# Optimization experiments

Measured on AMD Instinct MI355X. Metric: run time of the kernel, lower is better.

Reference implementation:

```python
import jax, jax.numpy as jnp
import numpy as np

B, S, K, N, G = 4, 16, 8192, 8192, 128
NUM_GROUPS = K // G

def setup_inputs() -> dict:
    key = jax.random.key(0)
    k1, k2, k3, k4, k5 = jax.random.split(key, 5)
    x = jax.random.normal(k1, (B, S, K), dtype=jnp.float32)
    qweight = jax.random.randint(k2, (K, N), -128, 128, dtype=jnp.int32)
    # small positive scales like real quantizers produce
    scales = jax.random.uniform(k3, (NUM_GROUPS, N), dtype=jnp.float32) * 0.01 + 1e-4
    zeros = jax.random.uniform(k4, (NUM_GROUPS, N), dtype=jnp.float32) * 2.0 - 1.0
    bias = jax.random.normal(k5, (N,), dtype=jnp.float32)
    return {"x": x, "qweight": qweight, "scales": scales, "zeros": zeros,
            "bias": bias, "group_size": G}

def reference(x, qweight, scales, zeros, bias, group_size):
    # Expand per-group scale/zero along K: [num_groups, N] -> [K, N]
    Kdim = qweight.shape[0]
    if scales.shape[0] == 1:
        scale_exp = jnp.broadcast_to(scales, (Kdim, scales.shape[1]))
        zero_exp = jnp.broadcast_to(zeros, (Kdim, zeros.shape[1]))
    else:
        scale_exp = jnp.repeat(scales, group_size, axis=0)[:Kdim]
        zero_exp = jnp.repeat(zeros, group_size, axis=0)[:Kdim]
    # Dequantize: W[k, n] = (q - zero) * scale
    weight_fp = (qweight.astype(x.dtype) - zero_exp) * scale_exp  # [K, N]
    out = jnp.einsum('bsk,kn->bsn', x, weight_fp) + bias
    return out
```

## Files before the change

kernel.cpp:

```cpp
#include <hip/hip_runtime.h>

typedef __attribute__((ext_vector_type(8))) short short8;
typedef __attribute__((ext_vector_type(8))) unsigned short ushort8;
typedef __attribute__((ext_vector_type(4))) unsigned short ushort4v;
typedef __attribute__((ext_vector_type(4))) int int4v;
typedef __attribute__((ext_vector_type(4))) float f32x4;

#define Mdim 64
#define Kdim 8192
#define Ndim 8192
#define GRP 128
#define NGRP 64
#define KSPLIT 8
#define NG2 (NGRP / KSPLIT)
#define BN 128

#define SWZ(row, kk) ((row)*128 + ((kk) ^ (8*((((row) >> 3) ^ (row)) & 7))))

__device__ __forceinline__ unsigned short f2bf(float f) {
    unsigned int u = __builtin_bit_cast(unsigned int, f);
    u += 0x7FFFu + ((u >> 16) & 1u);
    return (unsigned short)(u >> 16);
}
__device__ __forceinline__ float bf2f(unsigned short h) {
    unsigned int u = ((unsigned int)h) << 16;
    return __builtin_bit_cast(float, u);
}

__global__ void prep_kernel(const float* __restrict__ x,
                            unsigned short* __restrict__ xh,
                            unsigned short* __restrict__ xl,
                            float* __restrict__ xsum) {
    const int tid = threadIdx.x;
    const int u = blockIdx.x * 8 + (tid >> 5);
    const int g = u & (NGRP - 1);
    const int m = u >> 6;
    const int lane = tid & 31;
    const int k = g * GRP + lane * 4;
    f32x4 v = *(const f32x4*)(x + (size_t)m * Kdim + k);
    ushort4v hv, lv;
    float s = 0.f;
#pragma unroll
    for (int i = 0; i < 4; ++i) {
        unsigned short h = f2bf(v[i]);
        hv[i] = h;
        lv[i] = f2bf(v[i] - bf2f(h));
        s += v[i];
    }
    *(ushort4v*)(xh + (size_t)m * Kdim + k) = hv;
    *(ushort4v*)(xl + (size_t)m * Kdim + k) = lv;
#pragma unroll
    for (int off = 16; off > 0; off >>= 1) s += __shfl_down(s, off, 32);
    if (lane == 0) xsum[g * Mdim + m] = s;
}

__launch_bounds__(512, 4)
__global__ void qlin_kernel(const unsigned short* __restrict__ xh,
                            const unsigned short* __restrict__ xl,
                            const int* __restrict__ qw,
                            const float* __restrict__ scales,
                            const float* __restrict__ zeros,
                            const float* __restrict__ xsum,
                            float* __restrict__ pout) {
    __shared__ unsigned short lq[128 * 128];
    __shared__ unsigned short lxh[64 * 128];
    __shared__ unsigned short lxl[64 * 128];
    __shared__ float ls[NG2][128];
    __shared__ float lz[NG2][128];
    __shared__ float lxs[NG2][64];

    const int tid = threadIdx.x;
    const int kh = blockIdx.x & (KSPLIT - 1);
    const int n0 = (blockIdx.x >> 3) * BN;
    const int g0 = kh * NG2;
    const int ph = ((blockIdx.x >> 8) & 1) * (NG2 / 2);

    const int w = tid >> 6;
    const int l = tid & 63;
    const int lcol = l & 15;
    const int lhi = l >> 4;
    const int mt = (w >> 2) * 32;
    const int ns = (w & 3) * 32;

    const int qc = tid & 31;
    const int qr = tid >> 5;
    const int xc = tid & 15;
    const int xm = tid >> 4;

    const int c0 = n0 + ns + lcol;
    const int c1 = c0 + 16;

    int4v qv[8];
    ushort8 xga, xgb, xgc, xgd;

    auto LOADX = [&](int g) {
        const size_t kb = (size_t)g * GRP + xc * 8;
        xga = *(const ushort8*)(xh + (size_t)xm * Kdim + kb);
        xgb = *(const ushort8*)(xh + (size_t)(xm + 32) * Kdim + kb);
        xgc = *(const ushort8*)(xl + (size_t)xm * Kdim + kb);
        xgd = *(const ushort8*)(xl + (size_t)(xm + 32) * Kdim + kb);
    };
    auto LOADQ = [&](int g) {
        const size_t kb = (size_t)g * GRP + qr * 8;
        const int nc = n0 + qc * 4;
#pragma unroll
        for (int j = 0; j < 8; ++j)
            qv[j] = *(const int4v*)(qw + (kb + j) * Ndim + nc);
    };
    auto WRITEX = [&]() {
        *(ushort8*)&lxh[SWZ(xm, xc * 8)] = xga;
        *(ushort8*)&lxh[SWZ(xm + 32, xc * 8)] = xgb;
        *(ushort8*)&lxl[SWZ(xm, xc * 8)] = xgc;
        *(ushort8*)&lxl[SWZ(xm + 32, xc * 8)] = xgd;
    };
    auto WRITEQ = [&]() {
#pragma unroll
        for (int i = 0; i < 4; ++i) {
            int4v pk;
#pragma unroll
            for (int t = 0; t < 4; ++t) {
                unsigned lo = __builtin_bit_cast(unsigned, (float)qv[2 * t][i]) >> 16;
                unsigned hi = __builtin_bit_cast(unsigned, (float)qv[2 * t + 1][i]) & 0xFFFF0000u;
                pk[t] = (int)(lo | hi);
            }
            *(int4v*)&lq[SWZ(qc * 4 + i, qr * 8)] = pk;
        }
    };

    f32x4 acc00 = {0,0,0,0}, acc01 = {0,0,0,0}, acc10 = {0,0,0,0}, acc11 = {0,0,0,0};

    if (tid < 256) {
        *(f32x4*)&ls[tid >> 5][(tid & 31) * 4] =
            *(const f32x4*)(scales + (size_t)(g0 + (tid >> 5)) * Ndim + n0 + (tid & 31) * 4);
    } else {
        const int t = tid - 256;
        *(f32x4*)&lz[t >> 5][(t & 31) * 4] =
            *(const f32x4*)(zeros + (size_t)(g0 + (t >> 5)) * Ndim + n0 + (t & 31) * 4);
    }
    lxs[tid >> 6][tid & 63] = xsum[(g0 + (tid >> 6)) * Mdim + (tid & 63)];
    {
        const int ga = g0 + ph;
        LOADX(ga);
        LOADQ(ga);
        WRITEX();
        WRITEQ();
        __syncthreads();
    }

    for (int g = 0; g < NG2; ++g) {
        const int gi = (g + ph) & (NG2 - 1);
        const bool more = (g + 1 < NG2);

        if (more) {
            const int ga = g0 + ((g + 1 + ph) & (NG2 - 1));
            LOADX(ga);
            LOADQ(ga);
        }

        f32x4 p00 = {0,0,0,0}, p01 = {0,0,0,0}, p10 = {0,0,0,0}, p11 = {0,0,0,0};
#pragma unroll
        for (int ks = 0; ks < 4; ++ks) {
            const int kk = ks * 32 + lhi * 8;
            short8 bq0 = *(const short8*)&lq[SWZ(ns + lcol, kk)];
            short8 bq1 = *(const short8*)&lq[SWZ(ns + 16 + lcol, kk)];
            short8 ah0 = *(const short8*)&lxh[SWZ(mt + lcol, kk)];
            short8 al0 = *(const short8*)&lxl[SWZ(mt + lcol, kk)];
            short8 ah1 = *(const short8*)&lxh[SWZ(mt + 16 + lcol, kk)];
            short8 al1 = *(const short8*)&lxl[SWZ(mt + 16 + lcol, kk)];
            p00 = __builtin_amdgcn_mfma_f32_16x16x32_bf16(ah0, bq0, p00, 0, 0, 0);
            p00 = __builtin_amdgcn_mfma_f32_16x16x32_bf16(al0, bq0, p00, 0, 0, 0);
            p01 = __builtin_amdgcn_mfma_f32_16x16x32_bf16(ah0, bq1, p01, 0, 0, 0);
            p01 = __builtin_amdgcn_mfma_f32_16x16x32_bf16(al0, bq1, p01, 0, 0, 0);
            p10 = __builtin_amdgcn_mfma_f32_16x16x32_bf16(ah1, bq0, p10, 0, 0, 0);
            p10 = __builtin_amdgcn_mfma_f32_16x16x32_bf16(al1, bq0, p10, 0, 0, 0);
            p11 = __builtin_amdgcn_mfma_f32_16x16x32_bf16(ah1, bq1, p11, 0, 0, 0);
            p11 = __builtin_amdgcn_mfma_f32_16x16x32_bf16(al1, bq1, p11, 0, 0, 0);
        }
        {
            const float s0 = ls[gi][ns + lcol],      z0 = lz[gi][ns + lcol];
            const float s1 = ls[gi][ns + 16 + lcol], z1 = lz[gi][ns + 16 + lcol];
            f32x4 xs0 = *(const f32x4*)&lxs[gi][mt + lhi * 4];
            f32x4 xs1 = *(const f32x4*)&lxs[gi][mt + 16 + lhi * 4];
#pragma unroll
            for (int r = 0; r < 4; ++r) {
                acc00[r] += s0 * (p00[r] - z0 * xs0[r]);
                acc01[r] += s1 * (p01[r] - z1 * xs0[r]);
                acc10[r] += s0 * (p10[r] - z0 * xs1[r]);
                acc11[r] += s1 * (p11[r] - z1 * xs1[r]);
            }
        }

        if (more) {
            __syncthreads();
            WRITEX();
            WRITEQ();
            __syncthreads();
        }
    }

    const size_t ob = (size_t)kh * Mdim * Ndim;
#pragma unroll
    for (int r = 0; r < 4; ++r) {
        pout[ob + (size_t)(mt + lhi * 4 + r) * Ndim + c0] = acc00[r];
        pout[ob + (size_t)(mt + lhi * 4 + r) * Ndim + c1] = acc01[r];
        pout[ob + (size_t)(mt + 16 + lhi * 4 + r) * Ndim + c0] = acc10[r];
        pout[ob + (size_t)(mt + 16 + lhi * 4 + r) * Ndim + c1] = acc11[r];
    }
}

__global__ void reduce_kernel(const float* __restrict__ pout,
                              const float* __restrict__ bias,
                              float* __restrict__ out) {
    const size_t e = ((size_t)blockIdx.x * 256 + threadIdx.x) * 4;
    const int n = (int)(e & (Ndim - 1));
    f32x4 a = *(const f32x4*)(bias + n);
#pragma unroll
    for (int s = 0; s < KSPLIT; ++s) {
        f32x4 ppart = *(const f32x4*)(pout + (size_t)s * Mdim * Ndim + e);
#pragma unroll
        for (int r = 0; r < 4; ++r) a[r] += ppart[r];
    }
    *(f32x4*)(out + e) = a;
}

extern "C" void kernel_launch(void* const* d_in, const int* in_sizes, int n_in,
                              void* d_out, int out_size, void* d_ws, size_t ws_size,
                              hipStream_t stream) {
    const float* x = (const float*)d_in[0];
    const int* qw = (const int*)d_in[1];
    const float* scales = (const float*)d_in[2];
    const float* zeros = (const float*)d_in[3];
    const float* bias = (const float*)d_in[4];

    unsigned short* xh = (unsigned short*)d_ws;
    unsigned short* xl = xh + (size_t)Mdim * Kdim;
    float* xsum = (float*)(xl + (size_t)Mdim * Kdim);
    float* pout = xsum + NGRP * Mdim;
    float* out = (float*)d_out;

    prep_kernel<<<512, 256, 0, stream>>>(x, xh, xl, xsum);
    qlin_kernel<<<(Ndim / BN) * KSPLIT, 512, 0, stream>>>(xh, xl, qw, scales, zeros, xsum, pout);
    reduce_kernel<<<(Mdim * Ndim / 4) / 256, 256, 0, stream>>>(pout, bias, out);
}
```

Baseline: 61.53 us.

## Double-buffer LDS tiles with two-ahead prefetch and halve K-split

Shared-memory tiles for quantized weights and x hi/lo are now double-buffered, so each group step needs one barrier instead of two. Global loads for group g+2 are issued while group g+1 is written to the alternate buffer. KSPLIT drops from 8 to 4, which halves the partial-output traffic and the reduce work but gives each block twice as many K groups and half as many blocks. The per-block staggered start phase is removed, and launch bounds drop to 2 blocks per CU because LDS use roughly doubles, reducing occupancy.

```diff
diff --git a/kernel.cpp b/kernel.cpp
--- a/kernel.cpp
+++ b/kernel.cpp
@@ -11,7 +11,7 @@
 #define Ndim 8192
 #define GRP 128
 #define NGRP 64
-#define KSPLIT 8
+#define KSPLIT 4
 #define NG2 (NGRP / KSPLIT)
 #define BN 128
 
@@ -54,7 +54,7 @@
     if (lane == 0) xsum[g * Mdim + m] = s;
 }
 
-__launch_bounds__(512, 4)
+__launch_bounds__(512, 2)
 __global__ void qlin_kernel(const unsigned short* __restrict__ xh,
                             const unsigned short* __restrict__ xl,
                             const int* __restrict__ qw,
@@ -62,18 +62,17 @@
                             const float* __restrict__ zeros,
                             const float* __restrict__ xsum,
                             float* __restrict__ pout) {
-    __shared__ unsigned short lq[128 * 128];
-    __shared__ unsigned short lxh[64 * 128];
-    __shared__ unsigned short lxl[64 * 128];
+    __shared__ unsigned short lq[2][128 * 128];
+    __shared__ unsigned short lxh[2][64 * 128];
+    __shared__ unsigned short lxl[2][64 * 128];
     __shared__ float ls[NG2][128];
     __shared__ float lz[NG2][128];
     __shared__ float lxs[NG2][64];
 
     const int tid = threadIdx.x;
     const int kh = blockIdx.x & (KSPLIT - 1);
-    const int n0 = (blockIdx.x >> 3) * BN;
+    const int n0 = (blockIdx.x >> 2) * BN;
     const int g0 = kh * NG2;
-    const int ph = ((blockIdx.x >> 8) & 1) * (NG2 / 2);
 
     const int w = tid >> 6;
     const int l = tid & 63;
@@ -107,13 +106,13 @@
         for (int j = 0; j < 8; ++j)
             qv[j] = *(const int4v*)(qw + (kb + j) * Ndim + nc);
     };
-    auto WRITEX = [&]() {
-        *(ushort8*)&lxh[SWZ(xm, xc * 8)] = xga;
-        *(ushort8*)&lxh[SWZ(xm + 32, xc * 8)] = xgb;
-        *(ushort8*)&lxl[SWZ(xm, xc * 8)] = xgc;
-        *(ushort8*)&lxl[SWZ(xm + 32, xc * 8)] = xgd;
-    };
-    auto WRITEQ = [&]() {
+    auto WRITEX = [&](int b) {
+        *(ushort8*)&lxh[b][SWZ(xm, xc * 8)] = xga;
+        *(ushort8*)&lxh[b][SWZ(xm + 32, xc * 8)] = xgb;
+        *(ushort8*)&lxl[b][SWZ(xm, xc * 8)] = xgc;
+        *(ushort8*)&lxl[b][SWZ(xm + 32, xc * 8)] = xgd;
+    };
+    auto WRITEQ = [&](int b) {
 #pragma unroll
         for (int i = 0; i < 4; ++i) {
             int4v pk;
@@ -123,50 +122,44 @@
                 unsigned hi = __builtin_bit_cast(unsigned, (float)qv[2 * t + 1][i]) & 0xFFFF0000u;
                 pk[t] = (int)(lo | hi);
             }
-            *(int4v*)&lq[SWZ(qc * 4 + i, qr * 8)] = pk;
+            *(int4v*)&lq[b][SWZ(qc * 4 + i, qr * 8)] = pk;
         }
     };
 
     f32x4 acc00 = {0,0,0,0}, acc01 = {0,0,0,0}, acc10 = {0,0,0,0}, acc11 = {0,0,0,0};
 
-    if (tid < 256) {
-        *(f32x4*)&ls[tid >> 5][(tid & 31) * 4] =
-            *(const f32x4*)(scales + (size_t)(g0 + (tid >> 5)) * Ndim + n0 + (tid & 31) * 4);
-    } else {
-        const int t = tid - 256;
-        *(f32x4*)&lz[t >> 5][(t & 31) * 4] =
-            *(const f32x4*)(zeros + (size_t)(g0 + (t >> 5)) * Ndim + n0 + (t & 31) * 4);
-    }
-    lxs[tid >> 6][tid & 63] = xsum[(g0 + (tid >> 6)) * Mdim + (tid & 63)];
     {
-        const int ga = g0 + ph;
-        LOADX(ga);
-        LOADQ(ga);
-        WRITEX();
-        WRITEQ();
-        __syncthreads();
+        const int tg = tid >> 5, tc = tid & 31;
+        f32x4 sv = *(const f32x4*)(scales + (size_t)(g0 + tg) * Ndim + n0 + tc * 4);
+        f32x4 zv = *(const f32x4*)(zeros + (size_t)(g0 + tg) * Ndim + n0 + tc * 4);
+        float x0 = xsum[(g0 + (tid >> 6)) * Mdim + (tid & 63)];
+        float x1 = xsum[(g0 + ((tid + 512) >> 6)) * Mdim + (tid & 63)];
+        LOADX(g0);
+        LOADQ(g0);
+        *(f32x4*)&ls[tg][tc * 4] = sv;
+        *(f32x4*)&lz[tg][tc * 4] = zv;
+        (&lxs[0][0])[tid] = x0;
+        (&lxs[0][0])[tid + 512] = x1;
+        WRITEX(0);
+        WRITEQ(0);
+        if (1 < NG2) { LOADX(g0 + 1); LOADQ(g0 + 1); }
+        asm volatile("s_waitcnt lgkmcnt(0)" ::: "memory");
+        __builtin_amdgcn_s_barrier();
     }
 
     for (int g = 0; g < NG2; ++g) {
-        const int gi = (g + ph) & (NG2 - 1);
-        const bool more = (g + 1 < NG2);
-
-        if (more) {
-            const int ga = g0 + ((g + 1 + ph) & (NG2 - 1));
-            LOADX(ga);
-            LOADQ(ga);
-        }
+        const int b = g & 1;
 
         f32x4 p00 = {0,0,0,0}, p01 = {0,0,0,0}, p10 = {0,0,0,0}, p11 = {0,0,0,0};
 #pragma unroll
         for (int ks = 0; ks < 4; ++ks) {
             const int kk = ks * 32 + lhi * 8;
-            short8 bq0 = *(const short8*)&lq[SWZ(ns + lcol, kk)];
-            short8 bq1 = *(const short8*)&lq[SWZ(ns + 16 + lcol, kk)];
-            short8 ah0 = *(const short8*)&lxh[SWZ(mt + lcol, kk)];
-            short8 al0 = *(const short8*)&lxl[SWZ(mt + lcol, kk)];
-            short8 ah1 = *(const short8*)&lxh[SWZ(mt + 16 + lcol, kk)];
-            short8 al1 = *(const short8*)&lxl[SWZ(mt + 16 + lcol, kk)];
+            short8 bq0 = *(const short8*)&lq[b][SWZ(ns + lcol, kk)];
+            short8 bq1 = *(const short8*)&lq[b][SWZ(ns + 16 + lcol, kk)];
+            short8 ah0 = *(const short8*)&lxh[b][SWZ(mt + lcol, kk)];
+            short8 al0 = *(const short8*)&lxl[b][SWZ(mt + lcol, kk)];
+            short8 ah1 = *(const short8*)&lxh[b][SWZ(mt + 16 + lcol, kk)];
+            short8 al1 = *(const short8*)&lxl[b][SWZ(mt + 16 + lcol, kk)];
             p00 = __builtin_amdgcn_mfma_f32_16x16x32_bf16(ah0, bq0, p00, 0, 0, 0);
             p00 = __builtin_amdgcn_mfma_f32_16x16x32_bf16(al0, bq0, p00, 0, 0, 0);
             p01 = __builtin_amdgcn_mfma_f32_16x16x32_bf16(ah0, bq1, p01, 0, 0, 0);
@@ -177,10 +170,10 @@
             p11 = __builtin_amdgcn_mfma_f32_16x16x32_bf16(al1, bq1, p11, 0, 0, 0);
         }
         {
-            const float s0 = ls[gi][ns + lcol],      z0 = lz[gi][ns + lcol];
-            const float s1 = ls[gi][ns + 16 + lcol], z1 = lz[gi][ns + 16 + lcol];
-            f32x4 xs0 = *(const f32x4*)&lxs[gi][mt + lhi * 4];
-            f32x4 xs1 = *(const f32x4*)&lxs[gi][mt + 16 + lhi * 4];
+            const float s0 = ls[g][ns + lcol],      z0 = lz[g][ns + lcol];
+            const float s1 = ls[g][ns + 16 + lcol], z1 = lz[g][ns + 16 + lcol];
+            f32x4 xs0 = *(const f32x4*)&lxs[g][mt + lhi * 4];
+            f32x4 xs1 = *(const f32x4*)&lxs[g][mt + 16 + lhi * 4];
 #pragma unroll
             for (int r = 0; r < 4; ++r) {
                 acc00[r] += s0 * (p00[r] - z0 * xs0[r]);
@@ -190,11 +183,19 @@
             }
         }
 
-        if (more) {
-            __syncthreads();
-            WRITEX();
-            WRITEQ();
-            __syncthreads();
+        if (g + 1 < NG2) {
+            WRITEX(b ^ 1);
+            if (g + 2 < NG2) {
+                LOADX(g0 + g + 2);
+                __builtin_amdgcn_sched_barrier(0);
+            }
+            WRITEQ(b ^ 1);
+            if (g + 2 < NG2) {
+                LOADQ(g0 + g + 2);
+                __builtin_amdgcn_sched_barrier(0);
+            }
+            asm volatile("s_waitcnt lgkmcnt(0)" ::: "memory");
+            __builtin_amdgcn_s_barrier();
         }
     }
 
```

Measured after the change: 56.23 us. 1.09x faster.
